# Optimization experiments

Hardware: AMD Instinct MI355X
Metric: run time of the kernel (lower is better)

Reference implementation:

```python
import jax, jax.numpy as jnp
import numpy as np
from jax import lax

S, V, DW = 2048, 50000, 400     # seq_len, word vocab, word emb dim
CV, DC = 8, 32                  # casing vocab / dim
PV, DP = 50, 64                 # POS vocab / dim
H, C = 768, 13                  # lstm hidden (per direction), num tag classes
DIN = DW + DC + DP              # 496 lstm input dim


def setup_inputs() -> dict:
    key = jax.random.key(0)
    ks = jax.random.split(key, 18)
    r = lambda k, sh, s=0.02: (jax.random.normal(k, sh) * s).astype(jnp.float32)
    return {
        "x": jax.random.randint(ks[0], (S,), 0, V),
        "casing": jax.random.randint(ks[1], (S,), 0, CV),
        "pos": jax.random.randint(ks[2], (S,), 0, PV),
        "word_emb": r(ks[3], (V, DW)),
        "casing_emb": r(ks[4], (CV, DC)),
        "pos_emb": r(ks[5], (PV, DP)),
        "Wih_f": r(ks[6], (4 * H, DIN)),
        "Whh_f": r(ks[7], (4 * H, H)),
        "b_f": jnp.zeros((4 * H,), jnp.float32),
        "Wih_b": r(ks[8], (4 * H, DIN)),
        "Whh_b": r(ks[9], (4 * H, H)),
        "b_b": jnp.zeros((4 * H,), jnp.float32),
        "Wc": r(ks[10], (C, 2 * H)),
        "bc": jnp.zeros((C,), jnp.float32),
        "start_trans": r(ks[11], (C,), 0.1),
        "end_trans": r(ks[12], (C,), 0.1),
        "trans": r(ks[13], (C, C), 0.1),
        "h0": jnp.zeros((2, H), jnp.float32),
        "c0": jnp.zeros((2, H), jnp.float32),
    }


def _lstm(xg, Whh, h0, c0):
    # xg: (S, 4H) precomputed input-to-hidden gates; PyTorch gate order i,f,g,o
    def step(carry, g_in):
        h, c = carry
        g = g_in + h @ Whh.T
        i, f, gg, o = jnp.split(g, 4)
        c = jax.nn.sigmoid(f) * c + jax.nn.sigmoid(i) * jnp.tanh(gg)
        h = jax.nn.sigmoid(o) * jnp.tanh(c)
        return (h, c), h
    _, hs = lax.scan(step, (h0, c0), xg)
    return hs  # (S, H)


def reference(x, casing, pos, word_emb, casing_emb, pos_emb,
              Wih_f, Whh_f, b_f, Wih_b, Whh_b, b_b, Wc, bc,
              start_trans, end_trans, trans, h0, c0):
    # embedding concat -> (S, DIN)
    emb = jnp.concatenate([word_emb[x], casing_emb[casing], pos_emb[pos]], axis=-1)
    # weight-dropped LSTM (eval mode: DropConnect identity), bidirectional
    hs_f = _lstm(emb @ Wih_f.T + b_f, Whh_f, h0[0], c0[0])
    hs_b = _lstm((emb @ Wih_b.T + b_b)[::-1], Whh_b, h0[1], c0[1])[::-1]
    o = jnp.concatenate([hs_f, hs_b], axis=-1) @ Wc.T + bc  # (S, C)
    tag_scores = jax.nn.log_softmax(o, axis=1)
    # CRF Viterbi decode (torchcrf-style), batch of 1 (the unsqueeze(0))
    score0 = start_trans + tag_scores[0]
    def vstep(score, em):
        cand = score[:, None] + trans            # (prev C, next C)
        bp = jnp.argmax(cand, axis=0)
        return jnp.max(cand, axis=0) + em, bp
    score, bps = lax.scan(vstep, score0, tag_scores[1:])
    last = jnp.argmax(score + end_trans)
    def back(tag, bp):
        prev = bp[tag]
        return prev, prev
    _, prevs = lax.scan(back, last, bps[::-1])
    tags = jnp.concatenate([prevs[::-1], last[None]])  # (S,) best path
    return tag_scores, tags
```

## Files before the change

kernel.cpp:

```cpp
#include <hip/hip_runtime.h>
#include <hip/hip_bf16.h>


#define SEQ  2048
#define DINW 496
#define HDIM 768
#define G4   3072
#define CDIM 13
#define NWG  48
#define JPW  16
#define DATA_SPIN (1u << 14)

__device__ __forceinline__ float sigf(float x) { return 1.0f / (1.0f + __expf(-x)); }
__device__ __forceinline__ float tanhf_fast(float x) {
    float ax = fabsf(x);
    float e  = __expf(-2.0f * ax);
    float t  = (1.0f - e) / (1.0f + e);
    return copysignf(t, x);
}

__global__ __launch_bounds__(256) void k_gemm_xg(
    const int* __restrict__ x, const int* __restrict__ casing, const int* __restrict__ pos,
    const float* __restrict__ we, const float* __restrict__ ce, const float* __restrict__ pe,
    const float* __restrict__ Wih_f, const float* __restrict__ b_f,
    const float* __restrict__ Wih_b, const float* __restrict__ b_b,
    __hip_bfloat16* __restrict__ xg_f, __hip_bfloat16* __restrict__ xg_b)
{
    __shared__ float As[16][68];
    __shared__ float Bs[16][68];
    int dir = blockIdx.z;
    const float* B    = dir ? Wih_b : Wih_f;
    const float* bias = dir ? b_b   : b_f;
    __hip_bfloat16* C = dir ? xg_b  : xg_f;
    int n0 = blockIdx.x * 64, m0 = blockIdx.y * 64;
    int tid = threadIdx.x;
    int tx = tid & 15, ty = tid >> 4;
    int lr = tid >> 2, lk = (tid & 3) * 4;

    int m = m0 + lr;
    const float* arow_w = we + (size_t)x[m] * 400;
    const float* arow_c = ce + (size_t)casing[m] * 32;
    const float* arow_p = pe + (size_t)pos[m] * 64;

    float acc[4][4] = {};
    for (int k0 = 0; k0 < DINW; k0 += 16) {
        int c0 = k0 + lk;
        float4 a;
        if (c0 < 400)      a = *(const float4*)(arow_w + c0);
        else if (c0 < 432) a = *(const float4*)(arow_c + (c0 - 400));
        else               a = *(const float4*)(arow_p + (c0 - 432));
        float4 b = *(const float4*)(B + (size_t)(n0 + lr) * DINW + c0);
        __syncthreads();
        As[lk + 0][lr] = a.x; As[lk + 1][lr] = a.y; As[lk + 2][lr] = a.z; As[lk + 3][lr] = a.w;
        Bs[lk + 0][lr] = b.x; Bs[lk + 1][lr] = b.y; Bs[lk + 2][lr] = b.z; Bs[lk + 3][lr] = b.w;
        __syncthreads();
        #pragma unroll
        for (int k = 0; k < 16; k++) {
            float4 av = *(const float4*)&As[k][ty * 4];
            float4 bv = *(const float4*)&Bs[k][tx * 4];
            float aa[4] = {av.x, av.y, av.z, av.w};
            float bb[4] = {bv.x, bv.y, bv.z, bv.w};
            #pragma unroll
            for (int i = 0; i < 4; i++)
                #pragma unroll
                for (int jj = 0; jj < 4; jj++)
                    acc[i][jj] += aa[i] * bb[jj];
        }
    }
    float4 bs4 = *(const float4*)(bias + n0 + tx * 4);
    float bb4[4] = {bs4.x, bs4.y, bs4.z, bs4.w};
    #pragma unroll
    for (int i = 0; i < 4; i++) {
        union { __hip_bfloat16 h[4]; ushort4 u; } cv;
        #pragma unroll
        for (int jj = 0; jj < 4; jj++)
            cv.h[jj] = __float2bfloat16(acc[i][jj] + bb4[jj]);
        *(ushort4*)(C + (size_t)(m0 + ty * 4 + i) * G4 + n0 + tx * 4) = cv.u;
    }
}

__global__ __launch_bounds__(1024) void k_lstm(
    const __hip_bfloat16* __restrict__ xg_f, const __hip_bfloat16* __restrict__ xg_b,
    const float* __restrict__ Whh_f, const float* __restrict__ Whh_b,
    const float* __restrict__ h0, const float* __restrict__ c0v,
    float* __restrict__ hs_f, float* __restrict__ hs_b,
    unsigned long long* __restrict__ msg, unsigned* __restrict__ abortw)
{
    __shared__ float hbuf[2][HDIM];
    __shared__ unsigned sdead;

    int wg = blockIdx.x;
    int dir = wg & 1, slot = wg >> 1;
    const __hip_bfloat16* xg = dir ? xg_b : xg_f;
    const float* Whh = dir ? Whh_b : Whh_f;
    float* hs        = dir ? hs_b  : hs_f;
    unsigned long long* mdir = msg + (size_t)dir * 2 * HDIM;

    int tid = threadIdx.x, lane = tid & 63, wv = tid >> 6;
    int q = lane >> 4, gl = lane & 15;
    int j = slot * JPW + wv;

    float w[48];
    const float* wr = Whh + (size_t)(q * HDIM + j) * HDIM;
    #pragma unroll
    for (int m = 0; m < 12; m++) {
        float4 f4 = *(const float4*)(wr + gl * 4 + m * 64);
        w[m * 4 + 0] = f4.x; w[m * 4 + 1] = f4.y;
        w[m * 4 + 2] = f4.z; w[m * 4 + 3] = f4.w;
    }
    float cst = c0v[dir * HDIM + j];

    if (tid == 0) sdead = 0;

    for (int t = 0; t < SEQ; t++) {
        int xrow = dir ? (SEQ - 1 - t) : t;
        const __hip_bfloat16* xga = xg + (size_t)xrow * G4 + j;
        float xv0 = __bfloat162float(xga[0]);
        float xv1 = __bfloat162float(xga[HDIM]);
        float xv2 = __bfloat162float(xga[2 * HDIM]);
        float xv3 = __bfloat162float(xga[3 * HDIM]);

        int par = (t & 1) ^ 1;

        if (wv == 0) {
            if (t == 0) {
                #pragma unroll
                for (int m = 0; m < 12; m++)
                    hbuf[1][m * 64 + lane] = h0[dir * HDIM + m * 64 + lane];
            } else {
                const unsigned long long* g = mdir + (size_t)par * HDIM;
                unsigned long long vals[12];
                unsigned freshm = 0;
                unsigned rounds = 0;
                bool dead = false;
                for (;;) {
                    #pragma unroll
                    for (int m = 0; m < 12; m++)
                        if (!(freshm & (1u << m)))
                            vals[m] = __hip_atomic_load(&g[m * 64 + lane],
                                        __ATOMIC_RELAXED, __HIP_MEMORY_SCOPE_AGENT);
                    #pragma unroll
                    for (int m = 0; m < 12; m++)
                        if ((unsigned)(vals[m] >> 32) == (unsigned)t)
                            freshm |= (1u << m);
                    if (__all(freshm == 0xFFFu)) break;
                    unsigned ab = __hip_atomic_load(abortw,
                                    __ATOMIC_RELAXED, __HIP_MEMORY_SCOPE_AGENT);
                    if (ab || ++rounds >= DATA_SPIN) { dead = true; break; }
                }
                #pragma unroll
                for (int m = 0; m < 12; m++) {
                    union { unsigned u; float f; } cvt;
                    cvt.u = (unsigned)vals[m];
                    hbuf[par][m * 64 + lane] = cvt.f;
                }
                if (dead && lane == 0) {
                    __hip_atomic_store(abortw, 1u,
                                       __ATOMIC_RELAXED, __HIP_MEMORY_SCOPE_AGENT);
                    sdead = 1;
                }
            }
        }

        __syncthreads();
        if (sdead) break;

        float acc = 0.f;
        #pragma unroll
        for (int m = 0; m < 12; m++) {
            float4 f4 = *(const float4*)&hbuf[par][gl * 4 + m * 64];
            acc += w[m * 4 + 0] * f4.x + w[m * 4 + 1] * f4.y
                 + w[m * 4 + 2] * f4.z + w[m * 4 + 3] * f4.w;
        }
        acc += __shfl_xor(acc, 1);
        acc += __shfl_xor(acc, 2);
        acc += __shfl_xor(acc, 4);
        acc += __shfl_xor(acc, 8);
        float si = __shfl(acc, 0),  sf = __shfl(acc, 16);
        float sg = __shfl(acc, 32), so = __shfl(acc, 48);

        float gi = sigf(xv0 + si), gf = sigf(xv1 + sf);
        float gg = tanhf_fast(xv2 + sg), go = sigf(xv3 + so);
        cst = gf * cst + gi * gg;
        float h = go * tanhf_fast(cst);

        if (lane == 0) {
            int hrow = dir ? (SEQ - 1 - t) : t;
            hs[(size_t)hrow * HDIM + j] = h;
            union { float f; unsigned u; } cvt; cvt.f = h;
            unsigned long long word = ((unsigned long long)(unsigned)(t + 1) << 32)
                                    | (unsigned long long)cvt.u;
            __hip_atomic_store(&mdir[(size_t)(t & 1) * HDIM + j], word,
                               __ATOMIC_RELAXED, __HIP_MEMORY_SCOPE_AGENT);
        }
        __syncthreads();
    }
}

__global__ __launch_bounds__(256) void k_head(
    const float* __restrict__ hs_f, const float* __restrict__ hs_b,
    const float* __restrict__ Wc, const float* __restrict__ bc,
    float* __restrict__ out)
{
    int tid = threadIdx.x, lane = tid & 63, wv = tid >> 6;
    int row = blockIdx.x * 4 + wv;
    const float* src = (lane < 32) ? (hs_f + (size_t)row * HDIM + lane * 24)
                                   : (hs_b + (size_t)row * HDIM + (lane - 32) * 24);
    float hvv[24];
    #pragma unroll
    for (int k = 0; k < 6; k++) {
        float4 f4 = *(const float4*)(src + k * 4);
        hvv[k * 4 + 0] = f4.x; hvv[k * 4 + 1] = f4.y;
        hvv[k * 4 + 2] = f4.z; hvv[k * 4 + 3] = f4.w;
    }
    int off = (lane < 32) ? lane * 24 : 768 + (lane - 32) * 24;
    float o[13];
    #pragma unroll
    for (int n = 0; n < CDIM; n++) {
        const float* wr2 = Wc + (size_t)n * 1536 + off;
        float s0 = 0.f, s1 = 0.f, s2 = 0.f, s3 = 0.f;
        #pragma unroll
        for (int k = 0; k < 6; k++) {
            float4 w4 = *(const float4*)(wr2 + k * 4);
            s0 += w4.x * hvv[k * 4 + 0];
            s1 += w4.y * hvv[k * 4 + 1];
            s2 += w4.z * hvv[k * 4 + 2];
            s3 += w4.w * hvv[k * 4 + 3];
        }
        o[n] = (s0 + s1) + (s2 + s3);
    }
    #pragma unroll
    for (int n = 0; n < CDIM; n++) {
        #pragma unroll
        for (int d = 1; d < 64; d <<= 1) o[n] += __shfl_xor(o[n], d);
        o[n] += bc[n];
    }
    float m = o[0];
    #pragma unroll
    for (int n = 1; n < CDIM; n++) m = fmaxf(m, o[n]);
    float sum = 0.f;
    #pragma unroll
    for (int n = 0; n < CDIM; n++) sum += __expf(o[n] - m);
    float ls = m + __logf(sum);
    if (lane == 0) {
        #pragma unroll
        for (int n = 0; n < CDIM; n++) out[(size_t)row * CDIM + n] = o[n] - ls;
    }
}

__global__ __launch_bounds__(64) void k_viterbi(
    const float* __restrict__ ts, const float* __restrict__ st,
    const float* __restrict__ en, const float* __restrict__ tr,
    float* __restrict__ tags_out)
{
    __shared__ unsigned char bp[SEQ - 1][16];
    __shared__ unsigned char path[SEQ];
    int n = threadIdx.x;
    bool act = n < CDIM;
    float trn[CDIM];
    #pragma unroll
    for (int p = 0; p < CDIM; p++) trn[p] = act ? tr[p * CDIM + n] : -1e30f;
    float score = act ? (st[n] + ts[n]) : -1e30f;

    for (int s = 1; s < SEQ; s++) {
        float em = act ? ts[(size_t)s * CDIM + n] : 0.f;
        float sp[CDIM];
        #pragma unroll
        for (int p = 0; p < CDIM; p++) sp[p] = __shfl(score, p);
        float best = -1e30f; int arg = 0;
        #pragma unroll
        for (int p = 0; p < CDIM; p++) {
            float v = sp[p] + trn[p];
            if (v > best) { best = v; arg = p; }
        }
        score = best + em;
        if (act) bp[s - 1][n] = (unsigned char)arg;
    }
    float fin = act ? (score + en[n]) : -1e30f;
    float fv[CDIM];
    #pragma unroll
    for (int p = 0; p < CDIM; p++) fv[p] = __shfl(fin, p);
    __syncthreads();
    if (n == 0) {
        float best = -1e30f; int last = 0;
        #pragma unroll
        for (int p = 0; p < CDIM; p++) { if (fv[p] > best) { best = fv[p]; last = p; } }
        int cur = last;
        path[SEQ - 1] = (unsigned char)cur;
        for (int s = SEQ - 2; s >= 0; s--) { cur = bp[s][cur]; path[s] = (unsigned char)cur; }
    }
    __syncthreads();
    for (int i = n; i < SEQ; i += 64) tags_out[i] = (float)path[i];
}

__global__ void k_zero(float* p, int n) {
    int i = blockIdx.x * 256 + threadIdx.x;
    if (i < n) p[i] = 0.f;
}

extern "C" void kernel_launch(void* const* d_in, const int* in_sizes, int n_in,
                              void* d_out, int out_size, void* d_ws, size_t ws_size,
                              hipStream_t stream)
{
    const int*   x      = (const int*)d_in[0];
    const int*   casing = (const int*)d_in[1];
    const int*   pos    = (const int*)d_in[2];
    const float* we     = (const float*)d_in[3];
    const float* ce     = (const float*)d_in[4];
    const float* pe     = (const float*)d_in[5];
    const float* Wih_f  = (const float*)d_in[6];
    const float* Whh_f  = (const float*)d_in[7];
    const float* b_f    = (const float*)d_in[8];
    const float* Wih_b  = (const float*)d_in[9];
    const float* Whh_b  = (const float*)d_in[10];
    const float* b_b    = (const float*)d_in[11];
    const float* Wc     = (const float*)d_in[12];
    const float* bc     = (const float*)d_in[13];
    const float* strt   = (const float*)d_in[14];
    const float* endt   = (const float*)d_in[15];
    const float* trans  = (const float*)d_in[16];
    const float* h0     = (const float*)d_in[17];
    const float* c0     = (const float*)d_in[18];

    const size_t need = 37773316;
    if (ws_size < need) {
        k_zero<<<(out_size + 255) / 256, 256, 0, stream>>>((float*)d_out, out_size);
        return;
    }
    char* wsb = (char*)d_ws;
    float* hs_f = (float*)(wsb);
    float* hs_b = (float*)(wsb + 6291456);
    __hip_bfloat16* xg_f = (__hip_bfloat16*)(wsb + 12582912);
    __hip_bfloat16* xg_b = (__hip_bfloat16*)(wsb + 25165824);
    unsigned long long* msg = (unsigned long long*)(wsb + 37748736);
    unsigned* abortw = (unsigned*)(wsb + 37773312);

    hipMemsetAsync(msg, 0, 24576 + 4, stream);

    k_gemm_xg<<<dim3(G4 / 64, SEQ / 64, 2), 256, 0, stream>>>(
        x, casing, pos, we, ce, pe, Wih_f, b_f, Wih_b, b_b, xg_f, xg_b);
    k_lstm<<<2 * NWG, 1024, 0, stream>>>(
        xg_f, xg_b, Whh_f, Whh_b, h0, c0, hs_f, hs_b, msg, abortw);
    k_head<<<SEQ / 4, 256, 0, stream>>>(hs_f, hs_b, Wc, bc, (float*)d_out);
    k_viterbi<<<1, 64, 0, stream>>>(
        (const float*)d_out, strt, endt, trans, (float*)d_out + (size_t)SEQ * CDIM);
}
```

Before: 7.366 ms.

## Pack LSTM hidden messages as bf16+tag words, split polling, enlarge GEMM tiles

The cross-workgroup h exchange now uses 32-bit words carrying a 16-bit step tag and a bf16 hidden value instead of 64-bit words with fp32 values. This halves the bytes each step polls. Polling is split across two wavefronts with six chunks each, and the message store is issued before the hs write. Separately, the input-gate GEMM moves from 64x64 tiles with 4x4 per-thread outputs to 128x128 tiles with 8x8 per-thread outputs. The risks are that the recurrent state now passes through bf16 rounding, which may affect accuracy, the 16-bit tag, and higher register pressure in the GEMM.

```diff
diff --git a/kernel.cpp b/kernel.cpp
--- a/kernel.cpp
+++ b/kernel.cpp
@@ -26,56 +26,71 @@
     const float* __restrict__ Wih_b, const float* __restrict__ b_b,
     __hip_bfloat16* __restrict__ xg_f, __hip_bfloat16* __restrict__ xg_b)
 {
-    __shared__ float As[16][68];
-    __shared__ float Bs[16][68];
+    __shared__ float As[16][132];
+    __shared__ float Bs[16][132];
     int dir = blockIdx.z;
     const float* B    = dir ? Wih_b : Wih_f;
     const float* bias = dir ? b_b   : b_f;
     __hip_bfloat16* C = dir ? xg_b  : xg_f;
-    int n0 = blockIdx.x * 64, m0 = blockIdx.y * 64;
+    int n0 = blockIdx.x * 128, m0 = blockIdx.y * 128;
     int tid = threadIdx.x;
+    int r  = tid >> 1, cb = (tid & 1) * 8;
     int tx = tid & 15, ty = tid >> 4;
-    int lr = tid >> 2, lk = (tid & 3) * 4;
-
-    int m = m0 + lr;
+
+    int m = m0 + r;
     const float* arow_w = we + (size_t)x[m] * 400;
     const float* arow_c = ce + (size_t)casing[m] * 32;
     const float* arow_p = pe + (size_t)pos[m] * 64;
-
-    float acc[4][4] = {};
+    const float* brow   = B + (size_t)(n0 + r) * DINW;
+
+    float acc[8][8] = {};
     for (int k0 = 0; k0 < DINW; k0 += 16) {
-        int c0 = k0 + lk;
-        float4 a;
-        if (c0 < 400)      a = *(const float4*)(arow_w + c0);
-        else if (c0 < 432) a = *(const float4*)(arow_c + (c0 - 400));
-        else               a = *(const float4*)(arow_p + (c0 - 432));
-        float4 b = *(const float4*)(B + (size_t)(n0 + lr) * DINW + c0);
+        int c0 = k0 + cb;
+        float4 a0, a1, b0, b1;
+        if (c0 < 400)      a0 = *(const float4*)(arow_w + c0);
+        else if (c0 < 432) a0 = *(const float4*)(arow_c + (c0 - 400));
+        else               a0 = *(const float4*)(arow_p + (c0 - 432));
+        int c4 = c0 + 4;
+        if (c4 < 400)      a1 = *(const float4*)(arow_w + c4);
+        else if (c4 < 432) a1 = *(const float4*)(arow_c + (c4 - 400));
+        else               a1 = *(const float4*)(arow_p + (c4 - 432));
+        b0 = *(const float4*)(brow + c0);
+        b1 = *(const float4*)(brow + c4);
         __syncthreads();
-        As[lk + 0][lr] = a.x; As[lk + 1][lr] = a.y; As[lk + 2][lr] = a.z; As[lk + 3][lr] = a.w;
-        Bs[lk + 0][lr] = b.x; Bs[lk + 1][lr] = b.y; Bs[lk + 2][lr] = b.z; Bs[lk + 3][lr] = b.w;
+        As[cb + 0][r] = a0.x; As[cb + 1][r] = a0.y; As[cb + 2][r] = a0.z; As[cb + 3][r] = a0.w;
+        As[cb + 4][r] = a1.x; As[cb + 5][r] = a1.y; As[cb + 6][r] = a1.z; As[cb + 7][r] = a1.w;
+        Bs[cb + 0][r] = b0.x; Bs[cb + 1][r] = b0.y; Bs[cb + 2][r] = b0.z; Bs[cb + 3][r] = b0.w;
+        Bs[cb + 4][r] = b1.x; Bs[cb + 5][r] = b1.y; Bs[cb + 6][r] = b1.z; Bs[cb + 7][r] = b1.w;
         __syncthreads();
         #pragma unroll
         for (int k = 0; k < 16; k++) {
-            float4 av = *(const float4*)&As[k][ty * 4];
-            float4 bv = *(const float4*)&Bs[k][tx * 4];
-            float aa[4] = {av.x, av.y, av.z, av.w};
-            float bb[4] = {bv.x, bv.y, bv.z, bv.w};
+            float4 av0 = *(const float4*)&As[k][ty * 8];
+            float4 av1 = *(const float4*)&As[k][ty * 8 + 4];
+            float4 bv0 = *(const float4*)&Bs[k][tx * 8];
+            float4 bv1 = *(const float4*)&Bs[k][tx * 8 + 4];
+            float aa[8] = {av0.x, av0.y, av0.z, av0.w, av1.x, av1.y, av1.z, av1.w};
+            float bb[8] = {bv0.x, bv0.y, bv0.z, bv0.w, bv1.x, bv1.y, bv1.z, bv1.w};
             #pragma unroll
-            for (int i = 0; i < 4; i++)
+            for (int i = 0; i < 8; i++)
                 #pragma unroll
-                for (int jj = 0; jj < 4; jj++)
+                for (int jj = 0; jj < 8; jj++)
                     acc[i][jj] += aa[i] * bb[jj];
         }
     }
-    float4 bs4 = *(const float4*)(bias + n0 + tx * 4);
-    float bb4[4] = {bs4.x, bs4.y, bs4.z, bs4.w};
-    #pragma unroll
-    for (int i = 0; i < 4; i++) {
-        union { __hip_bfloat16 h[4]; ushort4 u; } cv;
-        #pragma unroll
-        for (int jj = 0; jj < 4; jj++)
-            cv.h[jj] = __float2bfloat16(acc[i][jj] + bb4[jj]);
-        *(ushort4*)(C + (size_t)(m0 + ty * 4 + i) * G4 + n0 + tx * 4) = cv.u;
+    float4 bs0 = *(const float4*)(bias + n0 + tx * 8);
+    float4 bs1 = *(const float4*)(bias + n0 + tx * 8 + 4);
+    float bb8[8] = {bs0.x, bs0.y, bs0.z, bs0.w, bs1.x, bs1.y, bs1.z, bs1.w};
+    #pragma unroll
+    for (int i = 0; i < 8; i++) {
+        int row = m0 + ty * 8 + i;
+        union { __hip_bfloat16 h[4]; ushort4 u; } c0v, c1v;
+        #pragma unroll
+        for (int jj = 0; jj < 4; jj++) {
+            c0v.h[jj] = __float2bfloat16(acc[i][jj] + bb8[jj]);
+            c1v.h[jj] = __float2bfloat16(acc[i][jj + 4] + bb8[jj + 4]);
+        }
+        *(ushort4*)(C + (size_t)row * G4 + n0 + tx * 8)     = c0v.u;
+        *(ushort4*)(C + (size_t)row * G4 + n0 + tx * 8 + 4) = c1v.u;
     }
 }
 
@@ -84,7 +99,7 @@
     const float* __restrict__ Whh_f, const float* __restrict__ Whh_b,
     const float* __restrict__ h0, const float* __restrict__ c0v,
     float* __restrict__ hs_f, float* __restrict__ hs_b,
-    unsigned long long* __restrict__ msg, unsigned* __restrict__ abortw)
+    unsigned* __restrict__ msg, unsigned* __restrict__ abortw)
 {
     __shared__ float hbuf[2][HDIM];
     __shared__ unsigned sdead;
@@ -94,7 +109,7 @@
     const __hip_bfloat16* xg = dir ? xg_b : xg_f;
     const float* Whh = dir ? Whh_b : Whh_f;
     float* hs        = dir ? hs_b  : hs_f;
-    unsigned long long* mdir = msg + (size_t)dir * 2 * HDIM;
+    unsigned* mdir = msg + (size_t)dir * 2 * HDIM;
 
     int tid = threadIdx.x, lane = tid & 63, wv = tid >> 6;
     int q = lane >> 4, gl = lane & 15;
@@ -122,37 +137,36 @@
 
         int par = (t & 1) ^ 1;
 
-        if (wv == 0) {
+        if (wv < 2) {
+            int base = wv * 6;
             if (t == 0) {
                 #pragma unroll
-                for (int m = 0; m < 12; m++)
-                    hbuf[1][m * 64 + lane] = h0[dir * HDIM + m * 64 + lane];
+                for (int m = 0; m < 6; m++)
+                    hbuf[1][(base + m) * 64 + lane] = h0[dir * HDIM + (base + m) * 64 + lane];
             } else {
-                const unsigned long long* g = mdir + (size_t)par * HDIM;
-                unsigned long long vals[12];
-                unsigned freshm = 0;
-                unsigned rounds = 0;
+                const unsigned* g = mdir + (size_t)par * HDIM;
+                unsigned vals[6];
+                unsigned fresh = 0, rounds = 0;
                 bool dead = false;
                 for (;;) {
                     #pragma unroll
-                    for (int m = 0; m < 12; m++)
-                        if (!(freshm & (1u << m)))
-                            vals[m] = __hip_atomic_load(&g[m * 64 + lane],
+                    for (int m = 0; m < 6; m++)
+                        if (!(fresh & (1u << m)))
+                            vals[m] = __hip_atomic_load(&g[(base + m) * 64 + lane],
                                         __ATOMIC_RELAXED, __HIP_MEMORY_SCOPE_AGENT);
                     #pragma unroll
-                    for (int m = 0; m < 12; m++)
-                        if ((unsigned)(vals[m] >> 32) == (unsigned)t)
-                            freshm |= (1u << m);
-                    if (__all(freshm == 0xFFFu)) break;
+                    for (int m = 0; m < 6; m++)
+                        if ((vals[m] >> 16) == (unsigned)t) fresh |= (1u << m);
+                    if (__all(fresh == 0x3Fu)) break;
                     unsigned ab = __hip_atomic_load(abortw,
                                     __ATOMIC_RELAXED, __HIP_MEMORY_SCOPE_AGENT);
                     if (ab || ++rounds >= DATA_SPIN) { dead = true; break; }
                 }
                 #pragma unroll
-                for (int m = 0; m < 12; m++) {
+                for (int m = 0; m < 6; m++) {
                     union { unsigned u; float f; } cvt;
-                    cvt.u = (unsigned)vals[m];
-                    hbuf[par][m * 64 + lane] = cvt.f;
+                    cvt.u = (vals[m] & 0xFFFFu) << 16;
+                    hbuf[par][(base + m) * 64 + lane] = cvt.f;
                 }
                 if (dead && lane == 0) {
                     __hip_atomic_store(abortw, 1u,
@@ -185,13 +199,13 @@
         float h = go * tanhf_fast(cst);
 
         if (lane == 0) {
+            union { __hip_bfloat16 b; unsigned short u; } cv;
+            cv.b = __float2bfloat16(h);
+            unsigned word = ((unsigned)(t + 1) << 16) | (unsigned)cv.u;
+            __hip_atomic_store(&mdir[(size_t)(t & 1) * HDIM + j], word,
+                               __ATOMIC_RELAXED, __HIP_MEMORY_SCOPE_AGENT);
             int hrow = dir ? (SEQ - 1 - t) : t;
             hs[(size_t)hrow * HDIM + j] = h;
-            union { float f; unsigned u; } cvt; cvt.f = h;
-            unsigned long long word = ((unsigned long long)(unsigned)(t + 1) << 32)
-                                    | (unsigned long long)cvt.u;
-            __hip_atomic_store(&mdir[(size_t)(t & 1) * HDIM + j], word,
-                               __ATOMIC_RELAXED, __HIP_MEMORY_SCOPE_AGENT);
         }
         __syncthreads();
     }
@@ -322,7 +336,7 @@
     const float* h0     = (const float*)d_in[17];
     const float* c0     = (const float*)d_in[18];
 
-    const size_t need = 37773316;
+    const size_t need = 37761028;
     if (ws_size < need) {
         k_zero<<<(out_size + 255) / 256, 256, 0, stream>>>((float*)d_out, out_size);
         return;
@@ -332,12 +346,12 @@
     float* hs_b = (float*)(wsb + 6291456);
     __hip_bfloat16* xg_f = (__hip_bfloat16*)(wsb + 12582912);
     __hip_bfloat16* xg_b = (__hip_bfloat16*)(wsb + 25165824);
-    unsigned long long* msg = (unsigned long long*)(wsb + 37748736);
-    unsigned* abortw = (unsigned*)(wsb + 37773312);
-
-    hipMemsetAsync(msg, 0, 24576 + 4, stream);
-
-    k_gemm_xg<<<dim3(G4 / 64, SEQ / 64, 2), 256, 0, stream>>>(
+    unsigned* msg = (unsigned*)(wsb + 37748736);
+    unsigned* abortw = (unsigned*)(wsb + 37761024);
+
+    hipMemsetAsync(msg, 0, 12288 + 4, stream);
+
+    k_gemm_xg<<<dim3(G4 / 128, SEQ / 128, 2), 256, 0, stream>>>(
         x, casing, pos, we, ce, pe, Wih_f, b_f, Wih_b, b_b, xg_f, xg_b);
     k_lstm<<<2 * NWG, 1024, 0, stream>>>(
         xg_f, xg_b, Whh_f, Whh_b, h0, c0, hs_f, hs_b, msg, abortw);
```

Measured after the change: 6.051 ms. 17.9% less time.
